# Kernel tuning notes

Measured on AMD Instinct MI355X. Metric: run time of the kernel, lower is better.

## Reference

```python
import jax, jax.numpy as jnp
import numpy as np

B, S, H, I, L, NH = 1, 256, 384, 1536, 2, 8

def _gelu(x):
    return jax.nn.gelu(x, approximate=False)  # torch nn.GELU default = exact erf

def _ln(x, g, b, eps=1e-5):
    m = x.mean(-1, keepdims=True)
    v = jnp.var(x, axis=-1, keepdims=True)
    return (x - m) / jnp.sqrt(v + eps) * g + b

def _mha(x, Wqkv, bqkv, Wo, bo):
    b_, s_, h_ = x.shape
    d = h_ // NH
    qkv = x @ Wqkv.T + bqkv  # [B,S,3H]
    q, k, v = jnp.split(qkv, 3, axis=-1)
    sp = lambda t: t.reshape(b_, s_, NH, d).transpose(0, 2, 1, 3)  # [B,NH,S,d]
    q, k, v = sp(q), sp(k), sp(v)
    att = jax.nn.softmax(jnp.einsum('bhqd,bhkd->bhqk', q * (1.0 / np.sqrt(d)), k), axis=-1)
    o = jnp.einsum('bhqk,bhkd->bhqd', att, v).transpose(0, 2, 1, 3).reshape(b_, s_, h_)
    return o @ Wo.T + bo

def _forward(hidden_states, Wqkv, bqkv, Wo, bo, W1, b1, W2, b2, g1, be1, g2, be2,
             Wbil, bbil, Wc1, bc1, Wc2, bc2, Wih, bih, Whh, bhh, Wp1, bp1, Wp2, bp2,
             Wout, bout, reasoning_steps):
    x = hidden_states
    rstate = jnp.zeros((x.shape[0], x.shape[-1]), x.dtype)
    cprobs, conts = [], []
    for _ in range(reasoning_steps):
        # symbolic reasoning layers (eval mode: dropout off)
        for l in range(L):
            x = _ln(x + _mha(x, Wqkv[l], bqkv[l], Wo[l], bo[l]), g1[l], be1[l])
            ff = _gelu(x @ W1[l].T + b1[l]) @ W2[l].T + b2[l]
            x = _ln(x + ff, g2[l], be2[l])
        # contradiction detector: bilinear over all token pairs
        tmp = jnp.einsum('bix,oxy->bioy', x, Wbil)            # [B,S,H,H]
        inter = jnp.einsum('bioy,bjy->bijo', tmp, x) + bbil   # [B,S,S,H]
        h1 = _gelu(inter @ Wc1.T + bc1)                       # [B,S,S,H]
        logits = jnp.einsum('bijh,h->bij', h1, Wc2[0]) + bc2[0]
        cprobs.append(jax.nn.sigmoid(logits))
        # recursive reasoning controller (GRUCell on mean-pooled states)
        pooled = x.mean(axis=1)
        gi = pooled @ Wih.T + bih
        gh = rstate @ Whh.T + bhh
        ir, iz, inn = jnp.split(gi, 3, axis=-1)
        hr, hz, hn = jnp.split(gh, 3, axis=-1)
        r = jax.nn.sigmoid(ir + hr)
        z = jax.nn.sigmoid(iz + hz)
        n = jnp.tanh(inn + r * hn)
        rstate = (1.0 - z) * n + z * rstate
        conts.append(jax.nn.sigmoid(_gelu(rstate @ Wp1.T + bp1) @ Wp2[0] + bp2[0]))
    final = x @ Wout.T + bout
    return final, jnp.stack(cprobs), jnp.stack(conts)

def setup_inputs():
    key = jax.random.key(0)
    ks = iter(jax.random.split(key, 40))
    rn = lambda shape, s=0.02: jax.random.normal(next(ks), shape, jnp.float32) * s
    return {
        'hidden_states': jax.random.normal(next(ks), (B, S, H), jnp.float32),
        'Wqkv': rn((L, 3 * H, H)), 'bqkv': jnp.zeros((L, 3 * H)),
        'Wo': rn((L, H, H)), 'bo': jnp.zeros((L, H)),
        'W1': rn((L, I, H)), 'b1': jnp.zeros((L, I)),
        'W2': rn((L, H, I)), 'b2': jnp.zeros((L, H)),
        'g1': jnp.ones((L, H)), 'be1': jnp.zeros((L, H)),
        'g2': jnp.ones((L, H)), 'be2': jnp.zeros((L, H)),
        'Wbil': rn((H, H, H)), 'bbil': jnp.zeros((H,)),
        'Wc1': rn((H, H)), 'bc1': jnp.zeros((H,)),
        'Wc2': rn((1, H)), 'bc2': jnp.zeros((1,)),
        'Wih': rn((3 * H, H)), 'bih': jnp.zeros((3 * H,)),
        'Whh': rn((3 * H, H)), 'bhh': jnp.zeros((3 * H,)),
        'Wp1': rn((H, H)), 'bp1': jnp.zeros((H,)),
        'Wp2': rn((1, H)), 'bp2': jnp.zeros((1,)),
        'Wout': rn((H, H)), 'bout': jnp.zeros((H,)),
        'reasoning_steps': 2,
    }

def reference(hidden_states, Wqkv, bqkv, Wo, bo, W1, b1, W2, b2, g1, be1, g2, be2,
              Wbil, bbil, Wc1, bc1, Wc2, bc2, Wih, bih, Whh, bhh, Wp1, bp1, Wp2, bp2,
              Wout, bout, reasoning_steps):
    return _forward(hidden_states, Wqkv, bqkv, Wo, bo, W1, b1, W2, b2, g1, be1, g2, be2,
                    Wbil, bbil, Wc1, bc1, Wc2, bc2, Wih, bih, Whh, bhh, Wp1, bp1, Wp2, bp2,
                    Wout, bout, reasoning_steps)
```

## Files before the change

### kernel.cpp

```cpp
#include <hip/hip_runtime.h>

typedef __attribute__((ext_vector_type(4))) float f32x4;
typedef __attribute__((ext_vector_type(8))) short s16x8;

#define DEVI __device__ __forceinline__

DEVI float b2f(short s) {
  union { float f; unsigned u; } v; v.u = ((unsigned)(unsigned short)s) << 16; return v.f;
}
DEVI short f2b(float f) {
  union { float f; unsigned u; } v; v.f = f;
  unsigned u = v.u;
  u += 0x7FFFu + ((u >> 16) & 1u);
  return (short)(u >> 16);
}
DEVI float gelu_f(float x) { return 0.5f * x * (1.0f + erff(x * 0.70710678118f)); }
DEVI float sigm_f(float x) { return 1.0f / (1.0f + expf(-x)); }

DEVI void gld16(const short* g, const short* l) {
  __builtin_amdgcn_global_load_lds((const __attribute__((address_space(1))) void*)g,
                                   (__attribute__((address_space(3))) void*)l, 16, 0, 0);
}

template<bool BIAS, bool GELU_ACT, bool OUT_BF16>
__global__ __launch_bounds__(256)
void gemm_fast_k(const short* __restrict__ A, const short* __restrict__ B,
                 const float* __restrict__ bias, void* __restrict__ Cv,
                 int M, int N, int K,
                 long long sA, long long sB, long long sC)
{
  __shared__ short As[128 * 32];
  __shared__ short Bs[128 * 32];
  const int bz = blockIdx.z;
  const int n0 = blockIdx.x * 128;
  const int m0 = blockIdx.y * 128;
  const int t = threadIdx.x, lane = t & 63, wave = t >> 6;
  const int wm = wave >> 1, wn = wave & 1;
  const short* Ab = A + bz * sA;
  const short* Bb = B + bz * sB;
  const int srow = lane >> 2;
  const int scol = (lane & 3) * 8;

  f32x4 acc[4][4];
#pragma unroll
  for (int i = 0; i < 4; ++i)
#pragma unroll
    for (int j = 0; j < 4; ++j) acc[i][j] = f32x4{0.f, 0.f, 0.f, 0.f};

  const int fr = lane & 15, fs = lane >> 4;

  for (int k0 = 0; k0 < K; k0 += 32) {
#pragma unroll
    for (int q = 0; q < 2; ++q) {
      int c = wave * 2 + q;
      gld16(Ab + (long long)(m0 + c * 16 + srow) * K + k0 + scol, &As[c * 512]);
      gld16(Bb + (long long)(n0 + c * 16 + srow) * K + k0 + scol, &Bs[c * 512]);
    }
    __syncthreads();
    s16x8 af[4], bfv[4];
#pragma unroll
    for (int i = 0; i < 4; ++i) af[i]  = *(const s16x8*)&As[(wm * 64 + i * 16 + fr) * 32 + fs * 8];
#pragma unroll
    for (int j = 0; j < 4; ++j) bfv[j] = *(const s16x8*)&Bs[(wn * 64 + j * 16 + fr) * 32 + fs * 8];
#pragma unroll
    for (int i = 0; i < 4; ++i)
#pragma unroll
      for (int j = 0; j < 4; ++j)
        acc[i][j] = __builtin_amdgcn_mfma_f32_16x16x32_bf16(af[i], bfv[j], acc[i][j], 0, 0, 0);
    __syncthreads();
  }

#pragma unroll
  for (int i = 0; i < 4; ++i) {
    int rowb = m0 + wm * 64 + i * 16 + fs * 4;
#pragma unroll
    for (int j = 0; j < 4; ++j) {
      int col = n0 + wn * 64 + j * 16 + fr;
      float bb = BIAS ? bias[col] : 0.0f;
#pragma unroll
      for (int u = 0; u < 4; ++u) {
        float v = acc[i][j][u] + bb;
        if constexpr (GELU_ACT) v = gelu_f(v);
        long long off = bz * sC + (long long)(rowb + u) * N + col;
        if constexpr (OUT_BF16) ((short*)Cv)[off] = f2b(v);
        else                    ((float*)Cv)[off] = v;
      }
    }
  }
}

template<bool BIAS, bool GELU_ACT, bool OUT_BF16>
__global__ __launch_bounds__(256)
void gemm64_k(const short* __restrict__ A, const short* __restrict__ B,
              const float* __restrict__ bias, void* __restrict__ Cv,
              int M, int N, int K)
{
  __shared__ short As[64 * 32];
  __shared__ short Bs[64 * 32];
  const int n0 = blockIdx.x * 64;
  const int m0 = blockIdx.y * 64;
  const int t = threadIdx.x, lane = t & 63, wave = t >> 6;
  const int wm = wave >> 1, wn = wave & 1;
  const int srow = lane >> 2;
  const int scol = (lane & 3) * 8;
  const int fr = lane & 15, fs = lane >> 4;

  f32x4 acc[2][2];
#pragma unroll
  for (int i = 0; i < 2; ++i)
#pragma unroll
    for (int j = 0; j < 2; ++j) acc[i][j] = f32x4{0.f, 0.f, 0.f, 0.f};

  for (int k0 = 0; k0 < K; k0 += 32) {
    gld16(A + (long long)(m0 + wave * 16 + srow) * K + k0 + scol, &As[wave * 512]);
    gld16(B + (long long)(n0 + wave * 16 + srow) * K + k0 + scol, &Bs[wave * 512]);
    __syncthreads();
    s16x8 af[2], bfv[2];
#pragma unroll
    for (int i = 0; i < 2; ++i) af[i]  = *(const s16x8*)&As[(wm * 32 + i * 16 + fr) * 32 + fs * 8];
#pragma unroll
    for (int j = 0; j < 2; ++j) bfv[j] = *(const s16x8*)&Bs[(wn * 32 + j * 16 + fr) * 32 + fs * 8];
#pragma unroll
    for (int i = 0; i < 2; ++i)
#pragma unroll
      for (int j = 0; j < 2; ++j)
        acc[i][j] = __builtin_amdgcn_mfma_f32_16x16x32_bf16(af[i], bfv[j], acc[i][j], 0, 0, 0);
    __syncthreads();
  }

#pragma unroll
  for (int i = 0; i < 2; ++i) {
    int rowb = m0 + wm * 32 + i * 16 + fs * 4;
#pragma unroll
    for (int j = 0; j < 2; ++j) {
      int col = n0 + wn * 32 + j * 16 + fr;
      float bb = BIAS ? bias[col] : 0.0f;
#pragma unroll
      for (int u = 0; u < 4; ++u) {
        float v = acc[i][j][u] + bb;
        if constexpr (GELU_ACT) v = gelu_f(v);
        long long off = (long long)(rowb + u) * N + col;
        if constexpr (OUT_BF16) ((short*)Cv)[off] = f2b(v);
        else                    ((float*)Cv)[off] = v;
      }
    }
  }
}

__global__ __launch_bounds__(256)
void transpose_k(const float* __restrict__ W, short* __restrict__ WT)
{
  __shared__ short L[64 * 68];
  const int o  = blockIdx.z;
  const int x0 = blockIdx.x * 64, y0 = blockIdx.y * 64;
  const float* Wo = W  + (long long)o * 147456;
  short*      WTo = WT + (long long)o * 147456;
  const int t  = threadIdx.x;
  const int rr = t >> 4;
  const int cc = (t & 15) * 4;
#pragma unroll
  for (int q = 0; q < 4; ++q) {
    int xl = rr + 16 * q;
    float4 v = *(const float4*)(Wo + (x0 + xl) * 384 + y0 + cc);
    short4 p; p.x = f2b(v.x); p.y = f2b(v.y); p.z = f2b(v.z); p.w = f2b(v.w);
    *(short4*)&L[xl * 68 + cc] = p;
  }
  __syncthreads();
#pragma unroll
  for (int q = 0; q < 4; ++q) {
    int yl = rr + 16 * q;
    short4 p;
    p.x = L[(cc + 0) * 68 + yl];
    p.y = L[(cc + 1) * 68 + yl];
    p.z = L[(cc + 2) * 68 + yl];
    p.w = L[(cc + 3) * 68 + yl];
    *(short4*)(WTo + (y0 + yl) * 384 + x0 + cc) = p;
  }
}

__global__ __launch_bounds__(256)
void convw_k(const float* __restrict__ W, short* __restrict__ Wb, int n)
{
  int i = (blockIdx.x * 256 + threadIdx.x) * 4;
  if (i < n) {
    float4 v = *(const float4*)(W + i);
    short4 p; p.x = f2b(v.x); p.y = f2b(v.y); p.z = f2b(v.z); p.w = f2b(v.w);
    *(short4*)(Wb + i) = p;
  }
}

__global__ __launch_bounds__(256)
void attn_k(const float* __restrict__ qkv, short* __restrict__ outb)
{
  __shared__ short Ks[256 * 48];
  __shared__ short Vs[256 * 48];
  __shared__ float Ps[32][258];
  const int h  = blockIdx.y;
  const int q0 = blockIdx.x * 32;
  const int t = threadIdx.x, lane = t & 63, wave = t >> 6;
  for (int idx = t; idx < 256 * 48; idx += 256) {
    int j = idx / 48, d = idx - j * 48;
    Ks[idx] = f2b(qkv[j * 1152 + 384 + h * 48 + d]);
    Vs[idx] = f2b(qkv[j * 1152 + 768 + h * 48 + d]);
  }
  __syncthreads();
  const int part = lane & 7;
  const int rl   = wave * 8 + (lane >> 3);
  const int row  = q0 + rl;
  float q[48];
#pragma unroll
  for (int d = 0; d < 48; ++d) q[d] = qkv[row * 1152 + h * 48 + d] * 0.14433756729740644f;
  float mx = -1e30f;
  for (int jj = 0; jj < 32; ++jj) {
    int j = jj * 8 + part;
    float a = 0.f;
#pragma unroll
    for (int dd = 0; dd < 12; ++dd) {
      short4 kk = *(const short4*)&Ks[j * 48 + dd * 4];
      a += q[dd*4+0]*b2f(kk.x) + q[dd*4+1]*b2f(kk.y) + q[dd*4+2]*b2f(kk.z) + q[dd*4+3]*b2f(kk.w);
    }
    Ps[rl][j] = a;
    mx = fmaxf(mx, a);
  }
  mx = fmaxf(mx, __shfl_xor(mx, 1));
  mx = fmaxf(mx, __shfl_xor(mx, 2));
  mx = fmaxf(mx, __shfl_xor(mx, 4));
  float sum = 0.f;
  for (int jj = 0; jj < 32; ++jj) {
    int j = jj * 8 + part;
    float e = expf(Ps[rl][j] - mx);
    Ps[rl][j] = e;
    sum += e;
  }
  sum += __shfl_xor(sum, 1); sum += __shfl_xor(sum, 2); sum += __shfl_xor(sum, 4);
  const float inv = 1.f / sum;
  __syncthreads();
  float o[6] = {0.f, 0.f, 0.f, 0.f, 0.f, 0.f};
  const int vb = part * 6;
  for (int j = 0; j < 256; ++j) {
    float p = Ps[rl][j];
    int base = j * 48 + vb;
#pragma unroll
    for (int dd = 0; dd < 3; ++dd) {
      short2 vv = *(const short2*)&Vs[base + dd * 2];
      o[dd*2]   += p * b2f(vv.x);
      o[dd*2+1] += p * b2f(vv.y);
    }
  }
#pragma unroll
  for (int d = 0; d < 6; ++d) outb[row * 384 + h * 48 + vb + d] = f2b(o[d] * inv);
}

__global__ __launch_bounds__(128)
void ln_k(const float* __restrict__ x, const float* __restrict__ d,
          const float* __restrict__ g, const float* __restrict__ b,
          float* __restrict__ xo, short* __restrict__ xob)
{
  const int row = blockIdx.x, t = threadIdx.x;
  float v[3]; float s = 0.f, ss = 0.f;
#pragma unroll
  for (int i = 0; i < 3; ++i) {
    int c = t + 128 * i;
    float u = x[row * 384 + c] + d[row * 384 + c];
    v[i] = u; s += u; ss += u * u;
  }
#pragma unroll
  for (int m = 1; m < 64; m <<= 1) { s += __shfl_xor(s, m); ss += __shfl_xor(ss, m); }
  __shared__ float sh[4];
  if ((t & 63) == 0) { sh[(t >> 6) * 2] = s; sh[(t >> 6) * 2 + 1] = ss; }
  __syncthreads();
  s = sh[0] + sh[2]; ss = sh[1] + sh[3];
  float mean = s * (1.f / 384.f);
  float var  = ss * (1.f / 384.f) - mean * mean;
  float rstd = rsqrtf(var + 1e-5f);
#pragma unroll
  for (int i = 0; i < 3; ++i) {
    int c = t + 128 * i;
    float y = (v[i] - mean) * rstd * g[c] + b[c];
    xo[row * 384 + c]  = y;
    xob[row * 384 + c] = f2b(y);
  }
}

__global__ void init_k(const float* __restrict__ hs, float* __restrict__ x,
                       short* __restrict__ xb, float* __restrict__ rstate)
{
  int i = blockIdx.x * 256 + threadIdx.x;
  if (i < 98304) { float v = hs[i]; x[i] = v; xb[i] = f2b(v); }
  if (i < 384) rstate[i] = 0.f;
}

__global__ __launch_bounds__(256)
void logits_k(const short* __restrict__ h1, const float* __restrict__ Wc2,
              const float* __restrict__ bc2, float* __restrict__ outp)
{
  const int t = threadIdx.x, lane = t & 63, wave = t >> 6;
  const int row = blockIdx.x * 4 + wave;
  const short* hr = h1 + (long long)row * 384;
  float a = 0.f;
#pragma unroll
  for (int e = 0; e < 6; ++e) { int c = lane + 64 * e; a += b2f(hr[c]) * Wc2[c]; }
#pragma unroll
  for (int m = 1; m < 64; m <<= 1) a += __shfl_xor(a, m);
  if (lane == 0) outp[row] = sigm_f(a + bc2[0]);
}

__global__ __launch_bounds__(384)
void pool1_k(const float* __restrict__ x, float* __restrict__ partial)
{
  const int t = threadIdx.x, p = blockIdx.x;
  float s = 0.f;
  const float* xr = x + p * 32 * 384;
#pragma unroll 4
  for (int i = 0; i < 32; ++i) s += xr[i * 384 + t];
  partial[p * 384 + t] = s;
}

__global__ __launch_bounds__(256)
void gih_k(const float* __restrict__ Wih, const float* __restrict__ bih,
           const float* __restrict__ Whh, const float* __restrict__ bhh,
           const float* __restrict__ partial, const float* __restrict__ rstate,
           float* __restrict__ gi, float* __restrict__ gh)
{
  const int t = threadIdx.x, lane = t & 63, wave = t >> 6;
  const int r = blockIdx.x * 4 + wave;
  float a = 0.f, b = 0.f;
#pragma unroll
  for (int e = 0; e < 6; ++e) {
    int c = lane + 64 * e;
    float pc = 0.f;
#pragma unroll
    for (int p = 0; p < 8; ++p) pc += partial[p * 384 + c];
    pc *= (1.f / 256.f);
    a += Wih[r * 384 + c] * pc;
    b += Whh[r * 384 + c] * rstate[c];
  }
#pragma unroll
  for (int m = 1; m < 64; m <<= 1) { a += __shfl_xor(a, m); b += __shfl_xor(b, m); }
  if (lane == 0) { gi[r] = a + bih[r]; gh[r] = b + bhh[r]; }
}

__global__ __launch_bounds__(384)
void gru2_k(const float* __restrict__ gi, const float* __restrict__ gh,
            float* __restrict__ rstate, float* __restrict__ hnew)
{
  const int t = threadIdx.x;
  float r = sigm_f(gi[t] + gh[t]);
  float z = sigm_f(gi[384 + t] + gh[384 + t]);
  float n = tanhf(gi[768 + t] + r * gh[768 + t]);
  float h = (1.f - z) * n + z * rstate[t];
  rstate[t] = h;
  hnew[t] = h;
}

__global__ __launch_bounds__(256)
void p1_k(const float* __restrict__ Wp1, const float* __restrict__ bp1,
          const float* __restrict__ hnew, float* __restrict__ p1)
{
  const int t = threadIdx.x, lane = t & 63, wave = t >> 6;
  const int r = blockIdx.x * 4 + wave;
  float a = 0.f;
#pragma unroll
  for (int e = 0; e < 6; ++e) { int c = lane + 64 * e; a += Wp1[r * 384 + c] * hnew[c]; }
#pragma unroll
  for (int m = 1; m < 64; m <<= 1) a += __shfl_xor(a, m);
  if (lane == 0) p1[r] = gelu_f(a + bp1[r]);
}

__global__ __launch_bounds__(64)
void cont_k(const float* __restrict__ p1, const float* __restrict__ Wp2,
            const float* __restrict__ bp2, float* __restrict__ out_cont)
{
  const int lane = threadIdx.x;
  float a = 0.f;
#pragma unroll
  for (int e = 0; e < 6; ++e) { int c = lane + 64 * e; a += p1[c] * Wp2[c]; }
#pragma unroll
  for (int m = 1; m < 64; m <<= 1) a += __shfl_xor(a, m);
  if (lane == 0) out_cont[0] = sigm_f(a + bp2[0]);
}

extern "C" void kernel_launch(void* const* d_in, const int* in_sizes, int n_in,
                              void* d_out, int out_size, void* d_ws, size_t ws_size,
                              hipStream_t stream)
{
  const float* hs   = (const float*)d_in[0];
  const float* Wqkv = (const float*)d_in[1];
  const float* bqkv = (const float*)d_in[2];
  const float* Wo   = (const float*)d_in[3];
  const float* bo   = (const float*)d_in[4];
  const float* W1   = (const float*)d_in[5];
  const float* b1   = (const float*)d_in[6];
  const float* W2   = (const float*)d_in[7];
  const float* b2   = (const float*)d_in[8];
  const float* g1   = (const float*)d_in[9];
  const float* be1  = (const float*)d_in[10];
  const float* g2   = (const float*)d_in[11];
  const float* be2  = (const float*)d_in[12];
  const float* Wbil = (const float*)d_in[13];
  const float* bbil = (const float*)d_in[14];
  const float* Wc1  = (const float*)d_in[15];
  const float* bc1  = (const float*)d_in[16];
  const float* Wc2  = (const float*)d_in[17];
  const float* bc2  = (const float*)d_in[18];
  const float* Wih  = (const float*)d_in[19];
  const float* bih  = (const float*)d_in[20];
  const float* Whh  = (const float*)d_in[21];
  const float* bhh  = (const float*)d_in[22];
  const float* Wp1  = (const float*)d_in[23];
  const float* bp1  = (const float*)d_in[24];
  const float* Wp2  = (const float*)d_in[25];
  const float* bp2  = (const float*)d_in[26];
  const float* Wout = (const float*)d_in[27];
  const float* bout = (const float*)d_in[28];
  float* out = (float*)d_out;

  char* ws = (char*)d_ws;
  size_t off = 0;
  auto alloc = [&](size_t bytes) -> char* {
    char* p = ws + off; off += (bytes + 255) & ~(size_t)255; return p;
  };
  short* wbilT  = (short*)alloc(56623104ULL * 2);
  short* tmp    = (short*)alloc(256ULL * 147456 * 2);
  short* inter  = (short*)alloc(256ULL * 98304 * 2);
  float* x      = (float*)alloc(98304 * 4);
  short* xb     = (short*)alloc(98304 * 2);
  float* qkv    = (float*)alloc(294912 * 4);
  short* attnb  = (short*)alloc(98304 * 2);
  float* delta  = (float*)alloc(98304 * 4);
  short* ff1b   = (short*)alloc(393216 * 2);
  float* rstate = (float*)alloc(384 * 4);
  float* partial= (float*)alloc(8 * 384 * 4);
  float* gi     = (float*)alloc(1152 * 4);
  float* gh     = (float*)alloc(1152 * 4);
  float* hnew   = (float*)alloc(384 * 4);
  float* p1buf  = (float*)alloc(384 * 4);
  short* wc1b   = (short*)alloc(147456 * 2);
  short* wqkvb  = (short*)alloc(884736ULL * 2);
  short* wob    = (short*)alloc(294912ULL * 2);
  short* w1b    = (short*)alloc(1179648ULL * 2);
  short* w2b    = (short*)alloc(1179648ULL * 2);
  short* woutb  = (short*)alloc(147456 * 2);
  short* h1 = tmp;
  (void)ws_size; (void)in_sizes; (void)n_in; (void)out_size;

  dim3 B256(256);

  init_k<<<dim3(384), B256, 0, stream>>>(hs, x, xb, rstate);
  transpose_k<<<dim3(6, 6, 384), B256, 0, stream>>>(Wbil, wbilT);
  convw_k<<<dim3(144),  B256, 0, stream>>>(Wc1, wc1b, 147456);
  convw_k<<<dim3(864),  B256, 0, stream>>>(Wqkv, wqkvb, 884736);
  convw_k<<<dim3(288),  B256, 0, stream>>>(Wo, wob, 294912);
  convw_k<<<dim3(1152), B256, 0, stream>>>(W1, w1b, 1179648);
  convw_k<<<dim3(1152), B256, 0, stream>>>(W2, w2b, 1179648);
  convw_k<<<dim3(144),  B256, 0, stream>>>(Wout, woutb, 147456);

  for (int s = 0; s < 2; ++s) {
    for (int l = 0; l < 2; ++l) {
      gemm64_k<true, false, false><<<dim3(18, 4), B256, 0, stream>>>(
          xb, wqkvb + l * 442368, bqkv + l * 1152, qkv, 256, 1152, 384);
      attn_k<<<dim3(8, 8), B256, 0, stream>>>(qkv, attnb);
      gemm64_k<true, false, false><<<dim3(6, 4), B256, 0, stream>>>(
          attnb, wob + l * 147456, bo + l * 384, delta, 256, 384, 384);
      ln_k<<<dim3(256), dim3(128), 0, stream>>>(x, delta, g1 + l * 384, be1 + l * 384, x, xb);
      gemm64_k<true, true, true><<<dim3(24, 4), B256, 0, stream>>>(
          xb, w1b + l * 589824, b1 + l * 1536, ff1b, 256, 1536, 384);
      gemm64_k<true, false, false><<<dim3(6, 4), B256, 0, stream>>>(
          ff1b, w2b + l * 589824, b2 + l * 384, delta, 256, 384, 1536);
      ln_k<<<dim3(256), dim3(128), 0, stream>>>(x, delta, g2 + l * 384, be2 + l * 384, x, xb);
    }
    gemm_fast_k<false, false, true><<<dim3(1152, 2, 1), B256, 0, stream>>>(
        xb, wbilT, (const float*)nullptr, tmp, 256, 147456, 384, 0, 0, 0);
    gemm_fast_k<true, false, true><<<dim3(3, 2, 256), B256, 0, stream>>>(
        xb, tmp, bbil, inter, 256, 384, 384, 0, 147456LL, 98304LL);
    gemm_fast_k<true, true, true><<<dim3(3, 2, 256), B256, 0, stream>>>(
        inter, wc1b, bc1, h1, 256, 384, 384, 98304LL, 0, 98304LL);
    logits_k<<<dim3(16384), B256, 0, stream>>>(h1, Wc2, bc2, out + 98304 + s * 65536);
    pool1_k<<<dim3(8), dim3(384), 0, stream>>>(x, partial);
    gih_k<<<dim3(288), B256, 0, stream>>>(Wih, bih, Whh, bhh, partial, rstate, gi, gh);
    gru2_k<<<dim3(1), dim3(384), 0, stream>>>(gi, gh, rstate, hnew);
    p1_k<<<dim3(96), B256, 0, stream>>>(Wp1, bp1, hnew, p1buf);
    cont_k<<<dim3(1), dim3(64), 0, stream>>>(p1buf, Wp2, bp2, out + 98304 + 131072 + s);
  }
  gemm64_k<true, false, false><<<dim3(6, 4), B256, 0, stream>>>(
      xb, woutb, bout, out, 256, 384, 384);
}
```

Measured before the change: 716.7 us.

## Fuse Wc1 GEMM with GELU and logit reduction; widen K tile with swizzled LDS

```diff
diff --git a/kernel.cpp b/kernel.cpp
--- a/kernel.cpp
+++ b/kernel.cpp
@@ -29,8 +29,8 @@
                  int M, int N, int K,
                  long long sA, long long sB, long long sC)
 {
-  __shared__ short As[128 * 32];
-  __shared__ short Bs[128 * 32];
+  __shared__ short As[128 * 64];
+  __shared__ short Bs[128 * 64];
   const int bz = blockIdx.z;
   const int n0 = blockIdx.x * 128;
   const int m0 = blockIdx.y * 128;
@@ -38,8 +38,9 @@
   const int wm = wave >> 1, wn = wave & 1;
   const short* Ab = A + bz * sA;
   const short* Bb = B + bz * sB;
-  const int srow = lane >> 2;
-  const int scol = (lane & 3) * 8;
+  const int srow = lane >> 3;
+  const int scol = ((lane & 7) ^ srow) * 8;
+  const int fr = lane & 15, fs = lane >> 4;
 
   f32x4 acc[4][4];
 #pragma unroll
@@ -47,26 +48,36 @@
 #pragma unroll
     for (int j = 0; j < 4; ++j) acc[i][j] = f32x4{0.f, 0.f, 0.f, 0.f};
 
-  const int fr = lane & 15, fs = lane >> 4;
-
-  for (int k0 = 0; k0 < K; k0 += 32) {
-#pragma unroll
-    for (int q = 0; q < 2; ++q) {
-      int c = wave * 2 + q;
-      gld16(Ab + (long long)(m0 + c * 16 + srow) * K + k0 + scol, &As[c * 512]);
-      gld16(Bb + (long long)(n0 + c * 16 + srow) * K + k0 + scol, &Bs[c * 512]);
+  for (int k0 = 0; k0 < K; k0 += 64) {
+#pragma unroll
+    for (int q = 0; q < 4; ++q) {
+      int c = wave * 4 + q;
+      gld16(Ab + (long long)(m0 + c * 8 + srow) * K + k0 + scol, &As[c * 512]);
+      gld16(Bb + (long long)(n0 + c * 8 + srow) * K + k0 + scol, &Bs[c * 512]);
     }
     __syncthreads();
-    s16x8 af[4], bfv[4];
-#pragma unroll
-    for (int i = 0; i < 4; ++i) af[i]  = *(const s16x8*)&As[(wm * 64 + i * 16 + fr) * 32 + fs * 8];
-#pragma unroll
-    for (int j = 0; j < 4; ++j) bfv[j] = *(const s16x8*)&Bs[(wn * 64 + j * 16 + fr) * 32 + fs * 8];
-#pragma unroll
-    for (int i = 0; i < 4; ++i)
-#pragma unroll
-      for (int j = 0; j < 4; ++j)
-        acc[i][j] = __builtin_amdgcn_mfma_f32_16x16x32_bf16(af[i], bfv[j], acc[i][j], 0, 0, 0);
+    s16x8 af[4][2], bfv[4][2];
+#pragma unroll
+    for (int i = 0; i < 4; ++i) {
+      int row = wm * 64 + i * 16 + fr;
+#pragma unroll
+      for (int s = 0; s < 2; ++s)
+        af[i][s] = *(const s16x8*)&As[row * 64 + (((s * 4 + fs) ^ (fr & 7)) * 8)];
+    }
+#pragma unroll
+    for (int j = 0; j < 4; ++j) {
+      int row = wn * 64 + j * 16 + fr;
+#pragma unroll
+      for (int s = 0; s < 2; ++s)
+        bfv[j][s] = *(const s16x8*)&Bs[row * 64 + (((s * 4 + fs) ^ (fr & 7)) * 8)];
+    }
+#pragma unroll
+    for (int s = 0; s < 2; ++s)
+#pragma unroll
+      for (int i = 0; i < 4; ++i)
+#pragma unroll
+        for (int j = 0; j < 4; ++j)
+          acc[i][j] = __builtin_amdgcn_mfma_f32_16x16x32_bf16(af[i][s], bfv[j][s], acc[i][j], 0, 0, 0);
     __syncthreads();
   }
 
@@ -87,6 +98,98 @@
       }
     }
   }
+}
+
+__global__ __launch_bounds__(256)
+void h1log_k(const short* __restrict__ inter, const short* __restrict__ Wc1b,
+             const float* __restrict__ bc1, const float* __restrict__ Wc2,
+             float* __restrict__ partial)
+{
+  __shared__ short As[128 * 64];
+  __shared__ short Bs[128 * 64];
+  __shared__ float part[128][2];
+  const int nt = blockIdx.x, jt = blockIdx.y, ib = blockIdx.z;
+  const int n0 = nt * 128, m0 = jt * 128;
+  const int t = threadIdx.x, lane = t & 63, wave = t >> 6;
+  const int wm = wave >> 1, wn = wave & 1;
+  const short* Ab = inter + (long long)ib * 98304;
+  const int srow = lane >> 3;
+  const int scol = ((lane & 7) ^ srow) * 8;
+  const int fr = lane & 15, fs = lane >> 4;
+
+  f32x4 acc[4][4];
+#pragma unroll
+  for (int i = 0; i < 4; ++i)
+#pragma unroll
+    for (int j = 0; j < 4; ++j) acc[i][j] = f32x4{0.f, 0.f, 0.f, 0.f};
+
+  for (int k0 = 0; k0 < 384; k0 += 64) {
+#pragma unroll
+    for (int q = 0; q < 4; ++q) {
+      int c = wave * 4 + q;
+      gld16(Ab + (long long)(m0 + c * 8 + srow) * 384 + k0 + scol, &As[c * 512]);
+      gld16(Wc1b + (long long)(n0 + c * 8 + srow) * 384 + k0 + scol, &Bs[c * 512]);
+    }
+    __syncthreads();
+    s16x8 af[4][2], bfv[4][2];
+#pragma unroll
+    for (int i = 0; i < 4; ++i) {
+      int row = wm * 64 + i * 16 + fr;
+#pragma unroll
+      for (int s = 0; s < 2; ++s)
+        af[i][s] = *(const s16x8*)&As[row * 64 + (((s * 4 + fs) ^ (fr & 7)) * 8)];
+    }
+#pragma unroll
+    for (int j = 0; j < 4; ++j) {
+      int row = wn * 64 + j * 16 + fr;
+#pragma unroll
+      for (int s = 0; s < 2; ++s)
+        bfv[j][s] = *(const s16x8*)&Bs[row * 64 + (((s * 4 + fs) ^ (fr & 7)) * 8)];
+    }
+#pragma unroll
+    for (int s = 0; s < 2; ++s)
+#pragma unroll
+      for (int i = 0; i < 4; ++i)
+#pragma unroll
+        for (int j = 0; j < 4; ++j)
+          acc[i][j] = __builtin_amdgcn_mfma_f32_16x16x32_bf16(af[i][s], bfv[j][s], acc[i][j], 0, 0, 0);
+    __syncthreads();
+  }
+
+  float lp[16];
+#pragma unroll
+  for (int e = 0; e < 16; ++e) lp[e] = 0.f;
+#pragma unroll
+  for (int i = 0; i < 4; ++i)
+#pragma unroll
+    for (int j = 0; j < 4; ++j) {
+      int col = n0 + wn * 64 + j * 16 + fr;
+      float w2 = Wc2[col], b1v = bc1[col];
+#pragma unroll
+      for (int u = 0; u < 4; ++u)
+        lp[i * 4 + u] += gelu_f(acc[i][j][u] + b1v) * w2;
+    }
+#pragma unroll
+  for (int m = 1; m < 16; m <<= 1)
+#pragma unroll
+    for (int e = 0; e < 16; ++e) lp[e] += __shfl_xor(lp[e], m);
+  if (fr == 0) {
+#pragma unroll
+    for (int e = 0; e < 16; ++e)
+      part[wm * 64 + (e >> 2) * 16 + fs * 4 + (e & 3)][wn] = lp[e];
+  }
+  __syncthreads();
+  if (t < 128)
+    partial[((long long)ib * 256 + m0 + t) * 4 + nt] = part[t][0] + part[t][1];
+}
+
+__global__ __launch_bounds__(256)
+void logits2_k(const float* __restrict__ partial, const float* __restrict__ bc2,
+               float* __restrict__ outp)
+{
+  int idx = blockIdx.x * 256 + threadIdx.x;
+  float v = partial[idx * 4] + partial[idx * 4 + 1] + partial[idx * 4 + 2] + bc2[0];
+  outp[idx] = sigm_f(v);
 }
 
 template<bool BIAS, bool GELU_ACT, bool OUT_BF16>
@@ -288,21 +391,6 @@
   int i = blockIdx.x * 256 + threadIdx.x;
   if (i < 98304) { float v = hs[i]; x[i] = v; xb[i] = f2b(v); }
   if (i < 384) rstate[i] = 0.f;
-}
-
-__global__ __launch_bounds__(256)
-void logits_k(const short* __restrict__ h1, const float* __restrict__ Wc2,
-              const float* __restrict__ bc2, float* __restrict__ outp)
-{
-  const int t = threadIdx.x, lane = t & 63, wave = t >> 6;
-  const int row = blockIdx.x * 4 + wave;
-  const short* hr = h1 + (long long)row * 384;
-  float a = 0.f;
-#pragma unroll
-  for (int e = 0; e < 6; ++e) { int c = lane + 64 * e; a += b2f(hr[c]) * Wc2[c]; }
-#pragma unroll
-  for (int m = 1; m < 64; m <<= 1) a += __shfl_xor(a, m);
-  if (lane == 0) outp[row] = sigm_f(a + bc2[0]);
 }
 
 __global__ __launch_bounds__(384)
@@ -420,28 +508,28 @@
   auto alloc = [&](size_t bytes) -> char* {
     char* p = ws + off; off += (bytes + 255) & ~(size_t)255; return p;
   };
-  short* wbilT  = (short*)alloc(56623104ULL * 2);
-  short* tmp    = (short*)alloc(256ULL * 147456 * 2);
-  short* inter  = (short*)alloc(256ULL * 98304 * 2);
-  float* x      = (float*)alloc(98304 * 4);
-  short* xb     = (short*)alloc(98304 * 2);
-  float* qkv    = (float*)alloc(294912 * 4);
-  short* attnb  = (short*)alloc(98304 * 2);
-  float* delta  = (float*)alloc(98304 * 4);
-  short* ff1b   = (short*)alloc(393216 * 2);
-  float* rstate = (float*)alloc(384 * 4);
-  float* partial= (float*)alloc(8 * 384 * 4);
-  float* gi     = (float*)alloc(1152 * 4);
-  float* gh     = (float*)alloc(1152 * 4);
-  float* hnew   = (float*)alloc(384 * 4);
-  float* p1buf  = (float*)alloc(384 * 4);
-  short* wc1b   = (short*)alloc(147456 * 2);
-  short* wqkvb  = (short*)alloc(884736ULL * 2);
-  short* wob    = (short*)alloc(294912ULL * 2);
-  short* w1b    = (short*)alloc(1179648ULL * 2);
-  short* w2b    = (short*)alloc(1179648ULL * 2);
-  short* woutb  = (short*)alloc(147456 * 2);
-  short* h1 = tmp;
+  short* wbilT   = (short*)alloc(56623104ULL * 2);
+  short* tmp     = (short*)alloc(256ULL * 147456 * 2);
+  short* inter   = (short*)alloc(256ULL * 98304 * 2);
+  float* x       = (float*)alloc(98304 * 4);
+  short* xb      = (short*)alloc(98304 * 2);
+  float* qkv     = (float*)alloc(294912 * 4);
+  short* attnb   = (short*)alloc(98304 * 2);
+  float* delta   = (float*)alloc(98304 * 4);
+  short* ff1b    = (short*)alloc(393216 * 2);
+  float* rstate  = (float*)alloc(384 * 4);
+  float* partial = (float*)alloc(8 * 384 * 4);
+  float* gi      = (float*)alloc(1152 * 4);
+  float* gh      = (float*)alloc(1152 * 4);
+  float* hnew    = (float*)alloc(384 * 4);
+  float* p1buf   = (float*)alloc(384 * 4);
+  short* wc1b    = (short*)alloc(147456 * 2);
+  short* wqkvb   = (short*)alloc(884736ULL * 2);
+  short* wob     = (short*)alloc(294912ULL * 2);
+  short* w1b     = (short*)alloc(1179648ULL * 2);
+  short* w2b     = (short*)alloc(1179648ULL * 2);
+  short* woutb   = (short*)alloc(147456 * 2);
+  float* lpart   = (float*)alloc(65536ULL * 4 * 4);
   (void)ws_size; (void)in_sizes; (void)n_in; (void)out_size;
 
   dim3 B256(256);
@@ -473,9 +561,8 @@
         xb, wbilT, (const float*)nullptr, tmp, 256, 147456, 384, 0, 0, 0);
     gemm_fast_k<true, false, true><<<dim3(3, 2, 256), B256, 0, stream>>>(
         xb, tmp, bbil, inter, 256, 384, 384, 0, 147456LL, 98304LL);
-    gemm_fast_k<true, true, true><<<dim3(3, 2, 256), B256, 0, stream>>>(
-        inter, wc1b, bc1, h1, 256, 384, 384, 98304LL, 0, 98304LL);
-    logits_k<<<dim3(16384), B256, 0, stream>>>(h1, Wc2, bc2, out + 98304 + s * 65536);
+    h1log_k<<<dim3(3, 2, 256), B256, 0, stream>>>(inter, wc1b, bc1, Wc2, lpart);
+    logits2_k<<<dim3(256), B256, 0, stream>>>(lpart, bc2, out + 98304 + s * 65536);
     pool1_k<<<dim3(8), dim3(384), 0, stream>>>(x, partial);
     gih_k<<<dim3(288), B256, 0, stream>>>(Wih, bih, Whh, bhh, partial, rstate, gi, gh);
     gru2_k<<<dim3(1), dim3(384), 0, stream>>>(gi, gh, rstate, hnew);
```

Result: slower. 768.1 us (+7.2%).
